# Performance work log

Measured on AMD Instinct MI355X. Metric: run time of the kernel, lower is better.

Reference implementation:

```python
import jax, jax.numpy as jnp
import numpy as np

HID = 2048
HEADS = 16
HD = HID // HEADS  # 128


def setup_inputs() -> dict:
    key = jax.random.key(0)
    ks = jax.random.split(key, 9)
    s = 0.02
    return {
        "hidden_state": jax.random.normal(ks[0], (2, 2048, HID), dtype=jnp.float32),
        "Wq": jax.random.normal(ks[1], (HID, HID), dtype=jnp.float32) * s,
        "bq": jnp.zeros((HID,), dtype=jnp.float32),
        "Wk": jax.random.normal(ks[2], (HID, HD), dtype=jnp.float32) * s,
        "bk": jnp.zeros((HD,), dtype=jnp.float32),
        "Wv": jax.random.normal(ks[3], (HID, HD), dtype=jnp.float32) * s,
        "bv": jnp.zeros((HD,), dtype=jnp.float32),
        "Wo": jax.random.normal(ks[4], (HID, HID), dtype=jnp.float32) * s,
        "bo": jnp.zeros((HID,), dtype=jnp.float32),
    }


def reference(hidden_state, Wq, bq, Wk, bk, Wv, bv, Wo, bo):
    bs, seq, _ = hidden_state.shape
    # Q: [b, s, H, hd] -> per-head; K,V: single shared head [b, s, hd]
    q = (hidden_state @ Wq + bq).reshape(bs, seq, HEADS, HD)
    k = hidden_state @ Wk + bk  # [b, s, hd]
    v = hidden_state @ Wv + bv  # [b, s, hd]
    scale = 1.0 / jnp.sqrt(jnp.float32(HD))
    # scores: [b, h, s_q, s_k] against shared K head
    scores = jnp.einsum("bqhd,bkd->bhqk", q, k) * scale
    attn = jax.nn.softmax(scores, axis=-1)
    out = jnp.einsum("bhqk,bkd->bqhd", attn, v)  # [b, s, h, hd]
    out = out.reshape(bs, seq, HID)
    return out @ Wo + bo
```

## Files before the change

### kernel.cpp

```cpp
#include <hip/hip_runtime.h>

#define HIDN 2048
#define NHEADS 16
#define HDIM 128
#define SEQ 2048
#define NB 2

typedef __bf16 bf16x8 __attribute__((ext_vector_type(8)));
typedef float f32x4 __attribute__((ext_vector_type(4)));

__device__ __forceinline__ unsigned short f32_to_bf16(float f) {
  unsigned int u = __float_as_uint(f);
  u += 0x7FFFu + ((u >> 16) & 1u);
  return (unsigned short)(u >> 16);
}

__device__ __forceinline__ void gload_lds16(const void* g, void* l) {
  __builtin_amdgcn_global_load_lds(
      (__attribute__((address_space(1))) void*)(g),
      (__attribute__((address_space(3))) void*)(l), 16, 0, 0);
}

__global__ __launch_bounds__(256) void cast_f32_bf16(
    const float* __restrict__ in, unsigned short* __restrict__ out, int n4) {
  int i = blockIdx.x * blockDim.x + threadIdx.x;
  if (i >= n4) return;
  float4 v = ((const float4*)in)[i];
  ushort4 o;
  o.x = f32_to_bf16(v.x); o.y = f32_to_bf16(v.y);
  o.z = f32_to_bf16(v.z); o.w = f32_to_bf16(v.w);
  ((ushort4*)out)[i] = o;
}

__global__ __launch_bounds__(256) void transpose_f32_bf16(
    const float* __restrict__ src, int srs,
    unsigned short* __restrict__ dst, int drs, int rows, int cols) {
  __shared__ float tile[32][33];
  int c0 = blockIdx.x * 32, r0 = blockIdx.y * 32;
  int tx = threadIdx.x & 31, ty = threadIdx.x >> 5;
#pragma unroll
  for (int i = 0; i < 32; i += 8)
    tile[ty + i][tx] = src[(size_t)(r0 + ty + i) * srs + c0 + tx];
  __syncthreads();
#pragma unroll
  for (int i = 0; i < 32; i += 8)
    dst[(size_t)(c0 + ty + i) * drs + r0 + tx] = f32_to_bf16(tile[tx][ty + i]);
}

__global__ __launch_bounds__(256) void transpose_bf16(
    const unsigned short* __restrict__ src, int srs,
    unsigned short* __restrict__ dst, int drs, int rows, int cols) {
  __shared__ unsigned short tile[32][33];
  int c0 = blockIdx.x * 32, r0 = blockIdx.y * 32;
  int tx = threadIdx.x & 31, ty = threadIdx.x >> 5;
#pragma unroll
  for (int i = 0; i < 32; i += 8)
    tile[ty + i][tx] = src[(size_t)(r0 + ty + i) * srs + c0 + tx];
  __syncthreads();
#pragma unroll
  for (int i = 0; i < 32; i += 8)
    dst[(size_t)(c0 + ty + i) * drs + r0 + tx] = tile[tx][ty + i];
}

__global__ __launch_bounds__(256) void concat_bias(
    const float* __restrict__ bq, const float* __restrict__ bk,
    const float* __restrict__ bv, float* __restrict__ out) {
  int i = blockIdx.x * blockDim.x + threadIdx.x;
  if (i >= 2304) return;
  out[i] = (i < 2048) ? bq[i] : ((i < 2176) ? bk[i - 2048] : bv[i - 2176]);
}

__global__ __launch_bounds__(256) void gemm_bt(
    const unsigned short* __restrict__ A,
    const unsigned short* __restrict__ BT,
    const float* __restrict__ bias,
    void* __restrict__ C, int K, int ldc, int outBf16) {
  __shared__ unsigned short As[128 * 64];
  __shared__ unsigned short Bs[128 * 64];
  const int tid = threadIdx.x;
  const int lane = tid & 63;
  const int wave = tid >> 6;
  const int wr = wave >> 1, wc = wave & 1;
  const int ml = lane & 15, quad = lane >> 4;
  const long bm = (long)blockIdx.x * 128;
  const long bn = (long)blockIdx.y * 128;

  const f32x4 zero4 = {0.f, 0.f, 0.f, 0.f};
  f32x4 acc[4][4];
#pragma unroll
  for (int mt = 0; mt < 4; ++mt)
#pragma unroll
    for (int nt = 0; nt < 4; ++nt) acc[mt][nt] = zero4;

  const int srow = lane >> 3;
  const int scol = ((lane & 7) ^ srow) * 8;

  for (int k0 = 0; k0 < K; k0 += 64) {
    __syncthreads();
#pragma unroll
    for (int r = 0; r < 4; ++r) {
      const int rowb = r * 32 + wave * 8;
      gload_lds16(A + (bm + rowb + srow) * (long)K + k0 + scol, &As[rowb * 64]);
      gload_lds16(BT + (bn + rowb + srow) * (long)K + k0 + scol, &Bs[rowb * 64]);
    }
    __syncthreads();
#pragma unroll
    for (int kk = 0; kk < 64; kk += 32) {
      const int g0 = (kk >> 3) + quad;
      bf16x8 af[4], bf[4];
#pragma unroll
      for (int mt = 0; mt < 4; ++mt)
        af[mt] = *(const bf16x8*)&As[(wr * 64 + mt * 16 + ml) * 64 +
                                     ((g0 ^ (ml & 7)) << 3)];
#pragma unroll
      for (int nt = 0; nt < 4; ++nt)
        bf[nt] = *(const bf16x8*)&Bs[(wc * 64 + nt * 16 + ml) * 64 +
                                     ((g0 ^ (ml & 7)) << 3)];
#pragma unroll
      for (int mt = 0; mt < 4; ++mt)
#pragma unroll
        for (int nt = 0; nt < 4; ++nt)
          acc[mt][nt] = __builtin_amdgcn_mfma_f32_16x16x32_bf16(
              af[mt], bf[nt], acc[mt][nt], 0, 0, 0);
    }
  }

#pragma unroll
  for (int mt = 0; mt < 4; ++mt) {
#pragma unroll
    for (int nt = 0; nt < 4; ++nt) {
      const long col = bn + wc * 64 + nt * 16 + ml;
      const float bval = bias ? bias[col] : 0.f;
#pragma unroll
      for (int r = 0; r < 4; ++r) {
        const long row = bm + wr * 64 + mt * 16 + quad * 4 + r;
        const float v = acc[mt][nt][r] + bval;
        if (outBf16)
          ((unsigned short*)C)[row * ldc + col] = f32_to_bf16(v);
        else
          ((float*)C)[row * ldc + col] = v;
      }
    }
  }
}

__global__ __launch_bounds__(256, 3) void mqa_attn(
    const unsigned short* __restrict__ qkv,
    const unsigned short* __restrict__ vt,
    unsigned short* __restrict__ outp) {
  __shared__ unsigned short Ks[64 * 128];
  __shared__ unsigned short VTs[128 * 64];
  __shared__ unsigned short Ps[64 * 72];

  const int tid = threadIdx.x;
  const int lane = tid & 63;
  const int wave = tid >> 6;
  const int ml = lane & 15, quad = lane >> 4;
  const int qt = blockIdx.x, h = blockIdx.y, b = blockIdx.z;
  const long q0 = (long)qt * 64;
  const long base = (long)b * SEQ;

  bf16x8 aq[4];
  {
    const unsigned short* qrow = qkv + (base + q0 + wave * 16 + ml) * 2304 + h * 128;
#pragma unroll
    for (int ks = 0; ks < 4; ++ks)
      aq[ks] = *(const bf16x8*)(qrow + ks * 32 + quad * 8);
  }

  const f32x4 zero4 = {0.f, 0.f, 0.f, 0.f};
  f32x4 o_acc[8];
#pragma unroll
  for (int nt = 0; nt < 8; ++nt) o_acc[nt] = zero4;
  float l_i[4] = {0.f, 0.f, 0.f, 0.f};
  const float scale = 0.08838834764831845f;

  const int srowK = lane >> 4;
  const int scolK = ((lane & 15) ^ (wave * 4 + srowK)) * 8;
  const int srowV = lane >> 3;
  const int scolV = ((lane & 7) ^ srowV) * 8;

  for (int kt = 0; kt < SEQ / 64; ++kt) {
    __syncthreads();
#pragma unroll
    for (int r = 0; r < 4; ++r) {
      const int rowb = r * 16 + wave * 4;
      gload_lds16(qkv + (base + kt * 64 + rowb + srowK) * 2304 + 2048 + scolK,
                  &Ks[rowb * 128]);
    }
#pragma unroll
    for (int r = 0; r < 4; ++r) {
      const int rowb = r * 32 + wave * 8;
      gload_lds16(vt + ((long)b * 128 + rowb + srowV) * SEQ + kt * 64 + scolV,
                  &VTs[rowb * 64]);
    }
    __syncthreads();

    f32x4 s[4];
#pragma unroll
    for (int nt = 0; nt < 4; ++nt) s[nt] = zero4;
#pragma unroll
    for (int ks = 0; ks < 4; ++ks) {
      const int g0 = ks * 4 + quad;
#pragma unroll
      for (int nt = 0; nt < 4; ++nt) {
        bf16x8 bk8 = *(const bf16x8*)&Ks[(nt * 16 + ml) * 128 + ((g0 ^ ml) << 3)];
        s[nt] = __builtin_amdgcn_mfma_f32_16x16x32_bf16(aq[ks], bk8, s[nt], 0, 0, 0);
      }
    }

#pragma unroll
    for (int nt = 0; nt < 4; ++nt)
#pragma unroll
      for (int r = 0; r < 4; ++r) {
        const float p = __expf(s[nt][r] * scale);
        l_i[r] += p;
        Ps[(wave * 16 + quad * 4 + r) * 72 + nt * 16 + ml] = f32_to_bf16(p);
      }

#pragma unroll
    for (int ks = 0; ks < 2; ++ks) {
      bf16x8 ap = *(const bf16x8*)&Ps[(wave * 16 + ml) * 72 + ks * 32 + quad * 8];
      const int g0 = ks * 4 + quad;
#pragma unroll
      for (int nt = 0; nt < 8; ++nt) {
        bf16x8 bv8 = *(const bf16x8*)&VTs[(nt * 16 + ml) * 64 + ((g0 ^ (ml & 7)) << 3)];
        o_acc[nt] = __builtin_amdgcn_mfma_f32_16x16x32_bf16(ap, bv8, o_acc[nt], 0, 0, 0);
      }
    }
  }

  float inv_l[4];
#pragma unroll
  for (int r = 0; r < 4; ++r) {
    float rs = l_i[r];
#pragma unroll
    for (int off = 1; off < 16; off <<= 1) rs += __shfl_xor(rs, off);
    inv_l[r] = 1.f / rs;
  }
#pragma unroll
  for (int nt = 0; nt < 8; ++nt)
#pragma unroll
    for (int r = 0; r < 4; ++r) {
      const long row = base + q0 + wave * 16 + quad * 4 + r;
      outp[row * HIDN + h * HDIM + nt * 16 + ml] =
          f32_to_bf16(o_acc[nt][r] * inv_l[r]);
    }
}

extern "C" void kernel_launch(void* const* d_in, const int* in_sizes, int n_in,
                              void* d_out, int out_size, void* d_ws, size_t ws_size,
                              hipStream_t stream) {
  const float* hidden = (const float*)d_in[0];
  const float* Wq = (const float*)d_in[1];
  const float* bq = (const float*)d_in[2];
  const float* Wk = (const float*)d_in[3];
  const float* bk = (const float*)d_in[4];
  const float* Wv = (const float*)d_in[5];
  const float* bv = (const float*)d_in[6];
  const float* Wo = (const float*)d_in[7];
  const float* bo = (const float*)d_in[8];
  float* out = (float*)d_out;

  char* ws = (char*)d_ws;
  const size_t MB = 1u << 20;
  unsigned short* hb    = (unsigned short*)(ws);
  unsigned short* attn  = hb;
  unsigned short* wqkvT = (unsigned short*)(ws + 16 * MB);
  unsigned short* woT   = (unsigned short*)(ws + 25 * MB);
  unsigned short* qkv   = (unsigned short*)(ws + 33 * MB);
  unsigned short* vt    = (unsigned short*)(ws + 51 * MB);
  float* biasqkv        = (float*)(ws + 52 * MB);

  cast_f32_bf16<<<8192, 256, 0, stream>>>(hidden, hb, (NB * SEQ * HIDN) / 4);
  transpose_f32_bf16<<<dim3(64, 64), 256, 0, stream>>>(Wq, 2048, wqkvT, 2048, 2048, 2048);
  transpose_f32_bf16<<<dim3(4, 64), 256, 0, stream>>>(Wk, 128, wqkvT + (size_t)2048 * 2048, 2048, 2048, 128);
  transpose_f32_bf16<<<dim3(4, 64), 256, 0, stream>>>(Wv, 128, wqkvT + (size_t)2176 * 2048, 2048, 2048, 128);
  transpose_f32_bf16<<<dim3(64, 64), 256, 0, stream>>>(Wo, 2048, woT, 2048, 2048, 2048);
  concat_bias<<<9, 256, 0, stream>>>(bq, bk, bv, biasqkv);

  gemm_bt<<<dim3(32, 18), 256, 0, stream>>>(hb, wqkvT, biasqkv, qkv, 2048, 2304, 1);

  transpose_bf16<<<dim3(4, 64), 256, 0, stream>>>(qkv + (size_t)0 * SEQ * 2304 + 2176, 2304, vt, 2048, 2048, 128);
  transpose_bf16<<<dim3(4, 64), 256, 0, stream>>>(qkv + (size_t)1 * SEQ * 2304 + 2176, 2304, vt + (size_t)128 * 2048, 2048, 2048, 128);

  mqa_attn<<<dim3(SEQ / 64, NHEADS, NB), 256, 0, stream>>>(qkv, vt, attn);

  gemm_bt<<<dim3(32, 16), 256, 0, stream>>>(attn, woT, bo, out, 2048, 2048, 0);
}
```

Before: 339.2 us.

## Merge prep kernels, retile QKV GEMM, swizzle P buffer and raise attention occupancy

Folds the four weight transposes and the bias concat into two launches, and the two V transposes into one launch, to cut kernel launch overhead. Templates the GEMM on N-tile width and uses 96-wide tiles for the QKV projection, giving 768 blocks instead of 576 for better wave balance across CUs. In attention it replaces the padded P buffer with an XOR-swizzled one, uses exp2f with a prescaled constant, hoists the K/V pointer arithmetic out of the loop, and raises the launch-bounds occupancy hint from 3 to 4. The tighter occupancy hint may force register spills.

```diff
diff --git a/kernel.cpp b/kernel.cpp
--- a/kernel.cpp
+++ b/kernel.cpp
@@ -1,4 +1,5 @@
 #include <hip/hip_runtime.h>
+#include <math.h>
 
 #define HIDN 2048
 #define NHEADS 16
@@ -32,65 +33,89 @@
   ((ushort4*)out)[i] = o;
 }
 
-__global__ __launch_bounds__(256) void transpose_f32_bf16(
-    const float* __restrict__ src, int srs,
-    unsigned short* __restrict__ dst, int drs, int rows, int cols) {
+__global__ __launch_bounds__(256) void wtrans_big(
+    const float* __restrict__ wq, unsigned short* __restrict__ dq,
+    const float* __restrict__ wo, unsigned short* __restrict__ do_) {
   __shared__ float tile[32][33];
+  const float* src = blockIdx.z ? wo : wq;
+  unsigned short* dst = blockIdx.z ? do_ : dq;
   int c0 = blockIdx.x * 32, r0 = blockIdx.y * 32;
   int tx = threadIdx.x & 31, ty = threadIdx.x >> 5;
 #pragma unroll
   for (int i = 0; i < 32; i += 8)
-    tile[ty + i][tx] = src[(size_t)(r0 + ty + i) * srs + c0 + tx];
+    tile[ty + i][tx] = src[(size_t)(r0 + ty + i) * 2048 + c0 + tx];
   __syncthreads();
 #pragma unroll
   for (int i = 0; i < 32; i += 8)
-    dst[(size_t)(c0 + ty + i) * drs + r0 + tx] = f32_to_bf16(tile[tx][ty + i]);
-}
-
-__global__ __launch_bounds__(256) void transpose_bf16(
-    const unsigned short* __restrict__ src, int srs,
-    unsigned short* __restrict__ dst, int drs, int rows, int cols) {
-  __shared__ unsigned short tile[32][33];
+    dst[(size_t)(c0 + ty + i) * 2048 + r0 + tx] = f32_to_bf16(tile[tx][ty + i]);
+}
+
+__global__ __launch_bounds__(256) void wtrans_small(
+    const float* __restrict__ wk, const float* __restrict__ wv,
+    unsigned short* __restrict__ dk, unsigned short* __restrict__ dv,
+    const float* __restrict__ bq, const float* __restrict__ bk,
+    const float* __restrict__ bv, float* __restrict__ biasout) {
+  __shared__ float tile[32][33];
+  const float* src = blockIdx.z ? wv : wk;
+  unsigned short* dst = blockIdx.z ? dv : dk;
   int c0 = blockIdx.x * 32, r0 = blockIdx.y * 32;
   int tx = threadIdx.x & 31, ty = threadIdx.x >> 5;
 #pragma unroll
   for (int i = 0; i < 32; i += 8)
-    tile[ty + i][tx] = src[(size_t)(r0 + ty + i) * srs + c0 + tx];
+    tile[ty + i][tx] = src[(size_t)(r0 + ty + i) * 128 + c0 + tx];
   __syncthreads();
 #pragma unroll
   for (int i = 0; i < 32; i += 8)
-    dst[(size_t)(c0 + ty + i) * drs + r0 + tx] = tile[tx][ty + i];
-}
-
-__global__ __launch_bounds__(256) void concat_bias(
-    const float* __restrict__ bq, const float* __restrict__ bk,
-    const float* __restrict__ bv, float* __restrict__ out) {
-  int i = blockIdx.x * blockDim.x + threadIdx.x;
-  if (i >= 2304) return;
-  out[i] = (i < 2048) ? bq[i] : ((i < 2176) ? bk[i - 2048] : bv[i - 2176]);
-}
-
+    dst[(size_t)(c0 + ty + i) * 2048 + r0 + tx] = f32_to_bf16(tile[tx][ty + i]);
+  if (blockIdx.z == 0) {
+    int lb = blockIdx.y * 4 + blockIdx.x;
+    if (lb < 9) {
+      int i = lb * 256 + threadIdx.x;
+      if (i < 2304)
+        biasout[i] = (i < 2048) ? bq[i] : ((i < 2176) ? bk[i - 2048] : bv[i - 2176]);
+    }
+  }
+}
+
+__global__ __launch_bounds__(256) void vtrans(
+    const unsigned short* __restrict__ qkv, unsigned short* __restrict__ vt) {
+  __shared__ unsigned short tile[32][33];
+  const unsigned short* src = qkv + (size_t)blockIdx.z * SEQ * 2304 + 2176;
+  unsigned short* dst = vt + (size_t)blockIdx.z * 128 * SEQ;
+  int c0 = blockIdx.x * 32, r0 = blockIdx.y * 32;
+  int tx = threadIdx.x & 31, ty = threadIdx.x >> 5;
+#pragma unroll
+  for (int i = 0; i < 32; i += 8)
+    tile[ty + i][tx] = src[(size_t)(r0 + ty + i) * 2304 + c0 + tx];
+  __syncthreads();
+#pragma unroll
+  for (int i = 0; i < 32; i += 8)
+    dst[(size_t)(c0 + ty + i) * SEQ + r0 + tx] = tile[tx][ty + i];
+}
+
+template <int BN>
 __global__ __launch_bounds__(256) void gemm_bt(
     const unsigned short* __restrict__ A,
     const unsigned short* __restrict__ BT,
     const float* __restrict__ bias,
     void* __restrict__ C, int K, int ldc, int outBf16) {
+  constexpr int NT = BN / 32;
   __shared__ unsigned short As[128 * 64];
-  __shared__ unsigned short Bs[128 * 64];
+  __shared__ unsigned short Bs[BN * 64];
   const int tid = threadIdx.x;
   const int lane = tid & 63;
   const int wave = tid >> 6;
   const int wr = wave >> 1, wc = wave & 1;
   const int ml = lane & 15, quad = lane >> 4;
   const long bm = (long)blockIdx.x * 128;
-  const long bn = (long)blockIdx.y * 128;
+  const long bn = (long)blockIdx.y * BN;
 
   const f32x4 zero4 = {0.f, 0.f, 0.f, 0.f};
-  f32x4 acc[4][4];
+  f32x4 acc[4][NT];
 #pragma unroll
   for (int mt = 0; mt < 4; ++mt)
 #pragma unroll
-    for (int nt = 0; nt < 4; ++nt) acc[mt][nt] = zero4;
+    for (int nt = 0; nt < NT; ++nt) acc[mt][nt] = zero4;
 
   const int srow = lane >> 3;
   const int scol = ((lane & 7) ^ srow) * 8;
@@ -101,25 +126,29 @@
     for (int r = 0; r < 4; ++r) {
       const int rowb = r * 32 + wave * 8;
       gload_lds16(A + (bm + rowb + srow) * (long)K + k0 + scol, &As[rowb * 64]);
+    }
+#pragma unroll
+    for (int r = 0; r < NT; ++r) {
+      const int rowb = r * 32 + wave * 8;
       gload_lds16(BT + (bn + rowb + srow) * (long)K + k0 + scol, &Bs[rowb * 64]);
     }
     __syncthreads();
 #pragma unroll
     for (int kk = 0; kk < 64; kk += 32) {
       const int g0 = (kk >> 3) + quad;
-      bf16x8 af[4], bf[4];
+      bf16x8 af[4], bf[NT];
 #pragma unroll
       for (int mt = 0; mt < 4; ++mt)
         af[mt] = *(const bf16x8*)&As[(wr * 64 + mt * 16 + ml) * 64 +
                                      ((g0 ^ (ml & 7)) << 3)];
 #pragma unroll
-      for (int nt = 0; nt < 4; ++nt)
-        bf[nt] = *(const bf16x8*)&Bs[(wc * 64 + nt * 16 + ml) * 64 +
+      for (int nt = 0; nt < NT; ++nt)
+        bf[nt] = *(const bf16x8*)&Bs[(wc * (BN / 2) + nt * 16 + ml) * 64 +
                                      ((g0 ^ (ml & 7)) << 3)];
 #pragma unroll
       for (int mt = 0; mt < 4; ++mt)
 #pragma unroll
-        for (int nt = 0; nt < 4; ++nt)
+        for (int nt = 0; nt < NT; ++nt)
           acc[mt][nt] = __builtin_amdgcn_mfma_f32_16x16x32_bf16(
               af[mt], bf[nt], acc[mt][nt], 0, 0, 0);
     }
@@ -128,8 +157,8 @@
 #pragma unroll
   for (int mt = 0; mt < 4; ++mt) {
 #pragma unroll
-    for (int nt = 0; nt < 4; ++nt) {
-      const long col = bn + wc * 64 + nt * 16 + ml;
+    for (int nt = 0; nt < NT; ++nt) {
+      const long col = bn + wc * (BN / 2) + nt * 16 + ml;
       const float bval = bias ? bias[col] : 0.f;
 #pragma unroll
       for (int r = 0; r < 4; ++r) {
@@ -144,13 +173,13 @@
   }
 }
 
-__global__ __launch_bounds__(256, 3) void mqa_attn(
+__global__ __launch_bounds__(256, 4) void mqa_attn(
     const unsigned short* __restrict__ qkv,
     const unsigned short* __restrict__ vt,
     unsigned short* __restrict__ outp) {
   __shared__ unsigned short Ks[64 * 128];
   __shared__ unsigned short VTs[128 * 64];
-  __shared__ unsigned short Ps[64 * 72];
+  __shared__ unsigned short Ps[64 * 64];
 
   const int tid = threadIdx.x;
   const int lane = tid & 63;
@@ -173,27 +202,29 @@
 #pragma unroll
   for (int nt = 0; nt < 8; ++nt) o_acc[nt] = zero4;
   float l_i[4] = {0.f, 0.f, 0.f, 0.f};
-  const float scale = 0.08838834764831845f;
+  const float c2 = 0.08838834764831845f * 1.4426950408889634f;
 
   const int srowK = lane >> 4;
   const int scolK = ((lane & 15) ^ (wave * 4 + srowK)) * 8;
   const int srowV = lane >> 3;
   const int scolV = ((lane & 7) ^ srowV) * 8;
+  const unsigned short* kp = qkv + (base + srowK) * 2304 + 2048 + scolK;
+  const unsigned short* vp = vt + ((long)b * 128 + srowV) * SEQ + scolV;
 
   for (int kt = 0; kt < SEQ / 64; ++kt) {
     __syncthreads();
 #pragma unroll
     for (int r = 0; r < 4; ++r) {
       const int rowb = r * 16 + wave * 4;
-      gload_lds16(qkv + (base + kt * 64 + rowb + srowK) * 2304 + 2048 + scolK,
-                  &Ks[rowb * 128]);
+      gload_lds16(kp + (long)rowb * 2304, &Ks[rowb * 128]);
     }
 #pragma unroll
     for (int r = 0; r < 4; ++r) {
       const int rowb = r * 32 + wave * 8;
-      gload_lds16(vt + ((long)b * 128 + rowb + srowV) * SEQ + kt * 64 + scolV,
-                  &VTs[rowb * 64]);
-    }
+      gload_lds16(vp + (long)rowb * SEQ, &VTs[rowb * 64]);
+    }
+    kp += 64 * 2304;
+    vp += 64;
     __syncthreads();
 
     f32x4 s[4];
@@ -213,15 +244,17 @@
     for (int nt = 0; nt < 4; ++nt)
 #pragma unroll
       for (int r = 0; r < 4; ++r) {
-        const float p = __expf(s[nt][r] * scale);
+        const float p = exp2f(s[nt][r] * c2);
         l_i[r] += p;
-        Ps[(wave * 16 + quad * 4 + r) * 72 + nt * 16 + ml] = f32_to_bf16(p);
+        const int pr = wave * 16 + quad * 4 + r;
+        const int g = nt * 2 + (ml >> 3);
+        Ps[pr * 64 + (((g ^ (pr & 7)) << 3) | (ml & 7))] = f32_to_bf16(p);
       }
 
 #pragma unroll
     for (int ks = 0; ks < 2; ++ks) {
-      bf16x8 ap = *(const bf16x8*)&Ps[(wave * 16 + ml) * 72 + ks * 32 + quad * 8];
       const int g0 = ks * 4 + quad;
+      bf16x8 ap = *(const bf16x8*)&Ps[(wave * 16 + ml) * 64 + ((g0 ^ (ml & 7)) << 3)];
 #pragma unroll
       for (int nt = 0; nt < 8; ++nt) {
         bf16x8 bv8 = *(const bf16x8*)&VTs[(nt * 16 + ml) * 64 + ((g0 ^ (ml & 7)) << 3)];
@@ -273,18 +306,16 @@
   float* biasqkv        = (float*)(ws + 52 * MB);
 
   cast_f32_bf16<<<8192, 256, 0, stream>>>(hidden, hb, (NB * SEQ * HIDN) / 4);
-  transpose_f32_bf16<<<dim3(64, 64), 256, 0, stream>>>(Wq, 2048, wqkvT, 2048, 2048, 2048);
-  transpose_f32_bf16<<<dim3(4, 64), 256, 0, stream>>>(Wk, 128, wqkvT + (size_t)2048 * 2048, 2048, 2048, 128);
-  transpose_f32_bf16<<<dim3(4, 64), 256, 0, stream>>>(Wv, 128, wqkvT + (size_t)2176 * 2048, 2048, 2048, 128);
-  transpose_f32_bf16<<<dim3(64, 64), 256, 0, stream>>>(Wo, 2048, woT, 2048, 2048, 2048);
-  concat_bias<<<9, 256, 0, stream>>>(bq, bk, bv, biasqkv);
-
-  gemm_bt<<<dim3(32, 18), 256, 0, stream>>>(hb, wqkvT, biasqkv, qkv, 2048, 2304, 1);
-
-  transpose_bf16<<<dim3(4, 64), 256, 0, stream>>>(qkv + (size_t)0 * SEQ * 2304 + 2176, 2304, vt, 2048, 2048, 128);
-  transpose_bf16<<<dim3(4, 64), 256, 0, stream>>>(qkv + (size_t)1 * SEQ * 2304 + 2176, 2304, vt + (size_t)128 * 2048, 2048, 2048, 128);
+  wtrans_big<<<dim3(64, 64, 2), 256, 0, stream>>>(Wq, wqkvT, Wo, woT);
+  wtrans_small<<<dim3(4, 64, 2), 256, 0, stream>>>(
+      Wk, Wv, wqkvT + (size_t)2048 * 2048, wqkvT + (size_t)2176 * 2048,
+      bq, bk, bv, biasqkv);
+
+  gemm_bt<96><<<dim3(32, 24), 256, 0, stream>>>(hb, wqkvT, biasqkv, qkv, 2048, 2304, 1);
+
+  vtrans<<<dim3(4, 64, 2), 256, 0, stream>>>(qkv, vt);
 
   mqa_attn<<<dim3(SEQ / 64, NHEADS, NB), 256, 0, stream>>>(qkv, vt, attn);
 
-  gemm_bt<<<dim3(32, 16), 256, 0, stream>>>(attn, woT, bo, out, 2048, 2048, 0);
-}
+  gemm_bt<128><<<dim3(32, 16), 256, 0, stream>>>(attn, woT, bo, out, 2048, 2048, 0);
+}
```

New measurement: 323.1 us. 1.05x faster.
